# Optimization experiments

Hardware: AMD Instinct MI355X
Metric: run time of the kernel (lower is better)

Reference implementation:

```python
import jax, jax.numpy as jnp
import numpy as np

B, C, H, W = 8, 256, 64, 64
NH = 8
CM = 2048
EPS = 1e-5


def setup_inputs() -> dict:
    key = jax.random.key(0)
    ks = jax.random.split(key, 16)
    n = lambda k, s: (jax.random.normal(k, s, dtype=jnp.float32) * 0.02)
    return {
        'x': jax.random.normal(ks[0], (B, C, H, W), dtype=jnp.float32),
        'Wqkv': n(ks[1], (C, 3 * C)), 'bqkv': n(ks[2], (3 * C,)),
        'dw_w': n(ks[3], (C, 1, 3, 3)), 'dw_b': n(ks[4], (C,)),
        'Wproj': n(ks[5], (C, C)), 'bproj': n(ks[6], (C,)),
        'bn1_g': jnp.ones((C,), jnp.float32), 'bn1_b': jnp.zeros((C,), jnp.float32),
        'bn1_m': n(ks[7], (C,)), 'bn1_v': jax.random.uniform(ks[8], (C,), dtype=jnp.float32) + 0.5,
        'alpha1': jnp.ones((1,), jnp.float32),
        'Wfc1': n(ks[9], (C, CM)), 'bfc1': n(ks[10], (CM,)),
        'Wfc2': n(ks[11], (CM, C)), 'bfc2': n(ks[12], (C,)),
        'bn2_g': jnp.ones((C,), jnp.float32), 'bn2_b': jnp.zeros((C,), jnp.float32),
        'bn2_m': n(ks[13], (C,)), 'bn2_v': jax.random.uniform(ks[14], (C,), dtype=jnp.float32) + 0.5,
        'alpha2': jnp.ones((1,), jnp.float32),
    }


def _repbn(x, g, b, m, v, alpha):
    # eval-mode RepBN: BatchNorm1d with running stats over channel dim + alpha*x
    bn = (x - m) * jax.lax.rsqrt(v + EPS) * g + b
    return bn + alpha * x


def reference(x, Wqkv, bqkv, dw_w, dw_b, Wproj, bproj,
              bn1_g, bn1_b, bn1_m, bn1_v, alpha1,
              Wfc1, bfc1, Wfc2, bfc2,
              bn2_g, bn2_b, bn2_m, bn2_v, alpha2):
    b, c, h, w = x.shape
    n = h * w
    hd = c // NH
    scale = hd ** (-0.5)
    t = x.reshape(b, c, n).transpose(0, 2, 1)  # [B,N,C]

    # --- SimplifiedLinearAttention ---
    qkv = (t @ Wqkv + bqkv).reshape(b, n, 3, NH, hd).transpose(2, 0, 3, 1, 4)
    q, k, v = qkv[0], qkv[1], qkv[2]          # [B,H,N,hd]
    q = jax.nn.relu(q) * scale
    k = jax.nn.relu(k)
    ctx = jnp.einsum('bhnd,bhne->bhde', k, v)  # [B,H,hd,hd] small context
    out = jnp.einsum('bhnd,bhde->bhne', q, ctx)
    out = out.transpose(0, 2, 1, 3).reshape(b, n, c)
    img = out.transpose(0, 2, 1).reshape(b, c, h, w)
    img = jax.lax.conv_general_dilated(img, dw_w, (1, 1), 'SAME',
                                       feature_group_count=c)
    img = img + dw_b[None, :, None, None]
    out = img.reshape(b, c, n).transpose(0, 2, 1)
    out = out @ Wproj + bproj

    # residual + RepBN (eval branch of LinearNorm)
    t = _repbn(t + out, bn1_g, bn1_b, bn1_m, bn1_v, alpha1)

    # FFN (exact GELU as nn.GELU default)
    ff = jax.nn.gelu(t @ Wfc1 + bfc1, approximate=False) @ Wfc2 + bfc2
    t = _repbn(t + ff, bn2_g, bn2_b, bn2_m, bn2_v, alpha2)

    return t.transpose(0, 2, 1).reshape(b, c, h, w)
```

## Files before the change

kernel.cpp:

```cpp
#include <hip/hip_runtime.h>
#include <hip/hip_bf16.h>
#include <math.h>

constexpr int B_ = 8, C_ = 256, H_ = 64, W_ = 64;
constexpr int N_ = H_ * W_;
constexpr int NH_ = 8;
constexpr int CM_ = 2048;
constexpr int M_ = B_ * N_;
constexpr float EPS_ = 1e-5f;

typedef __bf16 bf16_t;
typedef bf16_t bf16x4 __attribute__((ext_vector_type(4)));
typedef bf16_t bf16x8 __attribute__((ext_vector_type(8)));
typedef float f32x4 __attribute__((ext_vector_type(4)));

__device__ inline bf16_t f2b(float f) {
    __hip_bfloat16 h = __float2bfloat16(f);
    return *reinterpret_cast<bf16_t*>(&h);
}
__device__ inline float b2f(bf16_t b) {
    unsigned short u = *reinterpret_cast<unsigned short*>(&b);
    unsigned int x = (unsigned int)u << 16;
    return *reinterpret_cast<float*>(&x);
}
__device__ inline unsigned pk2(float lo, float hi) {
    bf16_t l = f2b(lo), h = f2b(hi);
    unsigned short ls = *reinterpret_cast<unsigned short*>(&l);
    unsigned short hs = *reinterpret_cast<unsigned short*>(&h);
    return ((unsigned)hs << 16) | (unsigned)ls;
}
__device__ inline float gelu_ap(float y) {
    float u = y * (0.7978845608f + 0.0356774081f * y * y);
    float e = __expf(2.0f * u);
    return y - y * __builtin_amdgcn_rcpf(e + 1.0f);
}

#define GLOAD_LDS16(gptr, lptr)                                                     \
    __builtin_amdgcn_global_load_lds(                                               \
        (const __attribute__((address_space(1))) void*)(gptr),                      \
        (__attribute__((address_space(3))) void*)(lptr), 16, 0, 0)

__global__ __launch_bounds__(256)
void prep(const float* __restrict__ x, bf16_t* __restrict__ t_b,
          const float* __restrict__ Wqkv, bf16_t* __restrict__ WqkvT,
          const float* __restrict__ Wproj, bf16_t* __restrict__ WprojT,
          const float* __restrict__ Wfc1, bf16_t* __restrict__ Wfc1T,
          const float* __restrict__ Wfc2, bf16_t* __restrict__ Wfc2T) {
    __shared__ float tile[32][33];
    int id = blockIdx.x;
    int tx = threadIdx.x, ty = threadIdx.y;

    const float* src;
    bf16_t* dst;
    int K, N, k0, n0;

    if (id < 8192) {
        int b = id >> 10, rem = id & 1023;
        int nn = (rem & 127) * 32, cc = (rem >> 7) * 32;
#pragma unroll
        for (int i = ty; i < 32; i += 8)
            tile[i][tx] = x[(size_t)b * C_ * N_ + (size_t)(cc + i) * N_ + nn + tx];
        __syncthreads();
#pragma unroll
        for (int i = ty; i < 32; i += 8)
            t_b[(size_t)b * N_ * C_ + (size_t)(nn + i) * C_ + cc + tx] = f2b(tile[tx][i]);
        return;
    } else if (id < 8384) {
        int idw = id - 8192; K = C_; N = 768;
        n0 = (idw % 24) * 32; k0 = (idw / 24) * 32;
        src = Wqkv; dst = WqkvT;
    } else if (id < 8448) {
        int idw = id - 8384; K = C_; N = C_;
        n0 = (idw & 7) * 32; k0 = (idw >> 3) * 32;
        src = Wproj; dst = WprojT;
    } else if (id < 8960) {
        int idw = id - 8448; K = C_; N = CM_;
        n0 = (idw & 63) * 32; k0 = (idw >> 6) * 32;
        src = Wfc1; dst = Wfc1T;
    } else {
        int idw = id - 8960; K = CM_; N = C_;
        n0 = (idw & 7) * 32; k0 = (idw >> 3) * 32;
        src = Wfc2; dst = Wfc2T;
    }
#pragma unroll
    for (int i = ty; i < 32; i += 8)
        tile[i][tx] = src[(size_t)(k0 + i) * N + n0 + tx];
    __syncthreads();
#pragma unroll
    for (int i = ty; i < 32; i += 8)
        dst[(size_t)(n0 + i) * K + k0 + tx] = f2b(tile[tx][i]);
}

template <int EPI>
__global__ __launch_bounds__(256, 4)
void gemm_swp(const bf16_t* __restrict__ Wt, const bf16_t* __restrict__ Act,
              const float* __restrict__ bias, bf16_t* __restrict__ Cb,
              int M, int N, int K,
              const bf16_t* __restrict__ tres_b,
              const float* __restrict__ g, const float* __restrict__ bb,
              const float* __restrict__ mm, const float* __restrict__ vv,
              const float* __restrict__ alpha) {
    __shared__ bf16x8 ldsv[2048];
    char* lds = (char*)ldsv;

    int tid  = threadIdx.x;
    int lane = tid & 63;
    int w    = tid >> 6;
    int wi   = w >> 1, wj = w & 1;

    int nwg = gridDim.x * gridDim.y;
    int bid = blockIdx.y * gridDim.x + blockIdx.x;
    int swz = (bid & 7) * (nwg >> 3) + (bid >> 3);
    int bx = swz % gridDim.x, by = swz / gridDim.x;
    int bch = bx * 128, bm = by * 128;

    int rowl = lane & 15, kq = lane >> 4;

    f32x4 acc[4][4] = {};

    for (int k0 = 0; k0 < K; k0 += 64) {
#pragma unroll
        for (int j = 0; j < 4; ++j) {
            int jj = w * 4 + j;
            int msub = jj >> 1, kh = jj & 1;
            const bf16_t* gw = Wt + ((size_t)(bch + msub * 16 + rowl) * K + k0 + kh * 32 + kq * 8);
            GLOAD_LDS16(gw, lds + jj * 1024);
            const bf16_t* ga = Act + ((size_t)(bm + msub * 16 + rowl) * K + k0 + kh * 32 + kq * 8);
            GLOAD_LDS16(ga, lds + 16384 + jj * 1024);
        }
        __syncthreads();
#pragma unroll
        for (int ks = 0; ks < 2; ++ks) {
            bf16x8 wf[4], af[4];
#pragma unroll
            for (int i = 0; i < 4; ++i) wf[i] = ldsv[((wi * 4 + i) * 2 + ks) * 64 + lane];
#pragma unroll
            for (int j = 0; j < 4; ++j) af[j] = ldsv[1024 + ((wj * 4 + j) * 2 + ks) * 64 + lane];
#pragma unroll
            for (int i = 0; i < 4; ++i)
#pragma unroll
                for (int j = 0; j < 4; ++j)
                    acc[i][j] = __builtin_amdgcn_mfma_f32_16x16x32_bf16(wf[i], af[j], acc[i][j], 0, 0, 0);
        }
        __syncthreads();
    }

    float alpha_v = (EPI == 1) ? alpha[0] : 0.f;
#pragma unroll
    for (int i = 0; i < 4; ++i) {
        int ch = bch + wi * 64 + i * 16 + (lane >> 4) * 4;
        f32x4 b4 = *(const f32x4*)(bias + ch);
        f32x4 rs4, B4, m4;
        if (EPI == 1) {
            f32x4 g4 = *(const f32x4*)(g + ch);
            f32x4 v4 = *(const f32x4*)(vv + ch);
            B4 = *(const f32x4*)(bb + ch);
            m4 = *(const f32x4*)(mm + ch);
#pragma unroll
            for (int r = 0; r < 4; ++r) rs4[r] = rsqrtf(v4[r] + EPS_) * g4[r];
        }
#pragma unroll
        for (int j = 0; j < 4; ++j) {
            int m = bm + wj * 64 + j * 16 + (lane & 15);
            f32x4 a = acc[i][j];
            bf16_t ob[4];
            if (EPI == 4) {
#pragma unroll
                for (int r = 0; r < 4; ++r) ob[r] = f2b(a[r] + b4[r]);
            } else {
                bf16x4 t4 = *(const bf16x4*)(tres_b + (size_t)m * N + ch);
#pragma unroll
                for (int r = 0; r < 4; ++r) {
                    float z = b2f(t4[r]) + a[r] + b4[r];
                    ob[r] = f2b((z - m4[r]) * rs4[r] + B4[r] + alpha_v * z);
                }
            }
            *(bf16x4*)(Cb + (size_t)m * N + ch) = *(bf16x4*)ob;
        }
    }
}

__global__ __launch_bounds__(512, 4)
void ffn_fused(const bf16_t* __restrict__ Act, const bf16_t* __restrict__ W1t,
               const bf16_t* __restrict__ W2t,
               const float* __restrict__ bfc1, const float* __restrict__ bfc2,
               const float* __restrict__ g, const float* __restrict__ bb,
               const float* __restrict__ mm, const float* __restrict__ vv,
               const float* __restrict__ alpha, float* __restrict__ out) {
    __shared__ char lds[65536];
    bf16x8* ldsA = (bf16x8*)lds;

    const int tid = threadIdx.x;
    const int lane = tid & 63;
    const int w = tid >> 6;
    const int l15 = lane & 15;
    const int kq = lane >> 4;
    const int m0 = blockIdx.x * 64;

#pragma unroll
    for (int j = 0; j < 4; ++j) {
        int jj = w * 4 + j;
        int mblk = jj >> 3, ks = jj & 7;
        const bf16_t* src = Act + (size_t)(m0 + mblk * 16 + l15) * 256 + ks * 32 + kq * 8;
        GLOAD_LDS16(src, lds + jj * 1024);
    }
    __syncthreads();

    f32x4 acc2[2][4] = {};

    const int hrow = w * 16 + l15;
    const int ks2w = w >> 1;
    const int lane2 = l15 + (((2 * w + (kq >> 1)) & 3) << 4);
    const int hwoff = (kq & 1) << 3;
    const int chb = w * 32;

    bf16x8 w1f[8];
#pragma unroll
    for (int ks = 0; ks < 8; ++ks)
        w1f[ks] = *(const bf16x8*)(W1t + (size_t)hrow * 256 + ks * 32 + kq * 8);

    for (int c = 0; c < 16; ++c) {
        f32x4 acc1[4] = {};
#pragma unroll
        for (int ks = 0; ks < 8; ++ks)
#pragma unroll
            for (int mblk = 0; mblk < 4; ++mblk)
                acc1[mblk] = __builtin_amdgcn_mfma_f32_16x16x32_bf16(
                    w1f[ks], ldsA[(mblk * 8 + ks) * 64 + lane], acc1[mblk], 0, 0, 0);

        if (c + 1 < 16) {
#pragma unroll
            for (int ks = 0; ks < 8; ++ks)
                w1f[ks] = *(const bf16x8*)(W1t + (size_t)((c + 1) * 128 + hrow) * 256 + ks * 32 + kq * 8);
        }
        bf16x8 w2f[2][4];
#pragma unroll
        for (int cf = 0; cf < 2; ++cf)
#pragma unroll
            for (int ks2 = 0; ks2 < 4; ++ks2)
                w2f[cf][ks2] = *(const bf16x8*)(W2t + (size_t)(chb + cf * 16 + l15) * 2048 + c * 128 + ks2 * 32 + kq * 8);

        f32x4 b1 = *(const f32x4*)(bfc1 + c * 128 + w * 16 + kq * 4);
        char* hbase = lds + 32768 + (c & 1) * 16384;
#pragma unroll
        for (int mblk = 0; mblk < 4; ++mblk) {
            uint2 u2;
            u2.x = pk2(gelu_ap(acc1[mblk][0] + b1[0]), gelu_ap(acc1[mblk][1] + b1[1]));
            u2.y = pk2(gelu_ap(acc1[mblk][2] + b1[2]), gelu_ap(acc1[mblk][3] + b1[3]));
            *(uint2*)(hbase + (size_t)((mblk * 4 + ks2w) * 64 + lane2) * 16 + hwoff) = u2;
        }
        __syncthreads();

        bf16x8* ldsH = (bf16x8*)(lds + 32768 + (c & 1) * 16384);
#pragma unroll
        for (int mblk = 0; mblk < 4; ++mblk)
#pragma unroll
            for (int ks2 = 0; ks2 < 4; ++ks2) {
                bf16x8 hf = ldsH[(mblk * 4 + ks2) * 64 + lane];
                acc2[0][mblk] = __builtin_amdgcn_mfma_f32_16x16x32_bf16(hf, w2f[0][ks2], acc2[0][mblk], 0, 0, 0);
                acc2[1][mblk] = __builtin_amdgcn_mfma_f32_16x16x32_bf16(hf, w2f[1][ks2], acc2[1][mblk], 0, 0, 0);
            }
    }

    float alpha_v = alpha[0];
#pragma unroll
    for (int cf = 0; cf < 2; ++cf) {
        int ch = chb + cf * 16 + l15;
        float b2v = bfc2[ch];
        float rs = rsqrtf(vv[ch] + EPS_) * g[ch];
        float bbv = bb[ch], mv = mm[ch];
#pragma unroll
        for (int mblk = 0; mblk < 4; ++mblk) {
            int mbase = m0 + mblk * 16 + kq * 4;
            f32x4 o4;
#pragma unroll
            for (int r = 0; r < 4; ++r) {
                float z = b2f(Act[(size_t)(mbase + r) * 256 + ch]) + acc2[cf][mblk][r] + b2v;
                o4[r] = (z - mv) * rs + bbv + alpha_v * z;
            }
            int bi = mbase >> 12, ni = mbase & (N_ - 1);
            *(f32x4*)(out + ((size_t)bi * C_ + ch) * N_ + ni) = o4;
        }
    }
}

__global__ void ctx_partial(const bf16_t* __restrict__ qkv, float* __restrict__ ctxp) {
    __shared__ float kb[64][40];
    __shared__ float vb[64][40];
    int seg = blockIdx.x;
    int bh  = blockIdx.y;
    int b = bh >> 3, h = bh & 7;
    int tid = threadIdx.x;
    int d  = tid >> 3;
    int e0 = (tid & 7) * 4;
    int lrow = tid >> 2, lcol = (tid & 3) * 8;
    float acc[4] = {0.f, 0.f, 0.f, 0.f};
    const size_t base = (size_t)b * N_ * 768 + h * 32;
    for (int n0 = seg * 512; n0 < seg * 512 + 512; n0 += 64) {
        size_t ra = base + (size_t)(n0 + lrow) * 768 + lcol;
        bf16x8 kv8 = *(const bf16x8*)(qkv + ra + 256);
        bf16x8 vv8 = *(const bf16x8*)(qkv + ra + 512);
#pragma unroll
        for (int j = 0; j < 8; ++j) {
            kb[lrow][lcol + j] = b2f(kv8[j]);
            vb[lrow][lcol + j] = b2f(vv8[j]);
        }
        __syncthreads();
#pragma unroll
        for (int nl = 0; nl < 64; ++nl) {
            float kv = fmaxf(kb[nl][d], 0.f);
#pragma unroll
            for (int j = 0; j < 4; ++j)
                acc[j] = fmaf(kv, vb[nl][e0 + j], acc[j]);
        }
        __syncthreads();
    }
    float* o = ctxp + ((size_t)seg * 64 + bh) * 1024 + d * 32 + e0;
#pragma unroll
    for (int j = 0; j < 4; ++j) o[j] = acc[j];
}

__global__ void attn_out(const bf16_t* __restrict__ qkv, const float* __restrict__ ctxp,
                         bf16_t* __restrict__ img) {
    __shared__ float qb[64][33];
    __shared__ float cs[32][32];
    int n0 = blockIdx.x * 64;
    int bh = blockIdx.y;
    int b = bh >> 3, h = bh & 7;
    int tid = threadIdx.x;
    const float scale = 0.17677669529663687f;
    {
        f32x4 vv = (f32x4)0.f;
#pragma unroll
        for (int seg = 0; seg < 8; ++seg) {
            f32x4 t = ((const f32x4*)(ctxp + ((size_t)seg * 64 + bh) * 1024))[tid];
            vv = vv + t;
        }
        ((f32x4*)&cs[0][0])[tid] = vv;
    }
    const size_t base = (size_t)b * N_ * 768 + h * 32;
    int lrow = tid >> 2, lcol = (tid & 3) * 8;
    {
        bf16x8 q8 = *(const bf16x8*)(qkv + base + (size_t)(n0 + lrow) * 768 + lcol);
#pragma unroll
        for (int j = 0; j < 8; ++j)
            qb[lrow][lcol + j] = fmaxf(b2f(q8[j]), 0.f) * scale;
    }
    __syncthreads();
    int nl = tid & 63, ebase = tid >> 6;
    bf16_t* outp = img + ((size_t)b * C_ + h * 32) * N_ + n0 + nl;
#pragma unroll
    for (int p = 0; p < 8; ++p) {
        int e = ebase + p * 4;
        float s = 0.f;
#pragma unroll
        for (int dd = 0; dd < 32; ++dd)
            s = fmaf(qb[nl][dd], cs[dd][e], s);
        outp[(size_t)e * N_] = f2b(s);
    }
}

__global__ __launch_bounds__(256)
void dwconvT(const bf16_t* __restrict__ img, const float* __restrict__ w,
             const float* __restrict__ bias, bf16_t* __restrict__ outb) {
    __shared__ float spf[3][32][66];
    __shared__ float otile[64][33];
    int id = blockIdx.x;
    int cg = id & 7, y = (id >> 3) & 63, b = id >> 9;
    int tid = threadIdx.x;
    int c_l = tid >> 3, xg = tid & 7;
    int c = cg * 32 + c_l;
    const bf16_t* ip = img + (size_t)(b * C_ + c) * N_;
#pragma unroll
    for (int dy = 0; dy < 3; ++dy) {
        int yy = y + dy - 1;
        if (yy < 0 || yy > 63) {
#pragma unroll
            for (int j = 0; j < 8; ++j) spf[dy][c_l][xg * 8 + j] = 0.f;
        } else {
            bf16x8 v8 = *(const bf16x8*)(ip + yy * 64 + xg * 8);
#pragma unroll
            for (int j = 0; j < 8; ++j) spf[dy][c_l][xg * 8 + j] = b2f(v8[j]);
        }
    }
    float wv[9];
#pragma unroll
    for (int j = 0; j < 9; ++j) wv[j] = w[c * 9 + j];
    float bv = bias[c];
    __syncthreads();

    float o[8];
#pragma unroll
    for (int i = 0; i < 8; ++i) o[i] = bv;
#pragma unroll
    for (int dy = 0; dy < 3; ++dy)
#pragma unroll
        for (int dx = -1; dx <= 1; ++dx) {
            float wgt = wv[dy * 3 + dx + 1];
#pragma unroll
            for (int i = 0; i < 8; ++i) {
                int xx = xg * 8 + i + dx;
                float val = (xx < 0 || xx > 63) ? 0.f : spf[dy][c_l][xx];
                o[i] = fmaf(wgt, val, o[i]);
            }
        }
#pragma unroll
    for (int i = 0; i < 8; ++i) otile[xg * 8 + i][c_l] = o[i];
    __syncthreads();

    int x_o = tid >> 2, cq = tid & 3;
    bf16_t ob[8];
#pragma unroll
    for (int j = 0; j < 8; ++j) ob[j] = f2b(otile[x_o][cq * 8 + j]);
    *(bf16x8*)(outb + ((size_t)b * N_ + y * 64 + x_o) * 256 + cg * 32 + cq * 8) = *(bf16x8*)&ob[0];
}

extern "C" void kernel_launch(void* const* d_in, const int* in_sizes, int n_in,
                              void* d_out, int out_size, void* d_ws, size_t ws_size,
                              hipStream_t stream) {
    const float* x     = (const float*)d_in[0];
    const float* Wqkv  = (const float*)d_in[1];
    const float* bqkv  = (const float*)d_in[2];
    const float* dw_w  = (const float*)d_in[3];
    const float* dw_b  = (const float*)d_in[4];
    const float* Wproj = (const float*)d_in[5];
    const float* bproj = (const float*)d_in[6];
    const float* bn1_g = (const float*)d_in[7];
    const float* bn1_b = (const float*)d_in[8];
    const float* bn1_m = (const float*)d_in[9];
    const float* bn1_v = (const float*)d_in[10];
    const float* alpha1= (const float*)d_in[11];
    const float* Wfc1  = (const float*)d_in[12];
    const float* bfc1  = (const float*)d_in[13];
    const float* Wfc2  = (const float*)d_in[14];
    const float* bfc2  = (const float*)d_in[15];
    const float* bn2_g = (const float*)d_in[16];
    const float* bn2_b = (const float*)d_in[17];
    const float* bn2_m = (const float*)d_in[18];
    const float* bn2_v = (const float*)d_in[19];
    const float* alpha2= (const float*)d_in[20];
    float* out = (float*)d_out;

    char* ws = (char*)d_ws;
    bf16_t* t_b2    = (bf16_t*)(ws);
    bf16_t* WqkvT   = (bf16_t*)(ws + 16777216);
    bf16_t* WprojT  = (bf16_t*)(ws + 17170432);
    bf16_t* Wfc1T   = (bf16_t*)(ws + 17301504);
    bf16_t* Wfc2T   = (bf16_t*)(ws + 18350080);
    float*  ctxp    = (float*)(ws + 19398656);
    bf16_t* t_b     = (bf16_t*)(ws + 21757952);
    bf16_t* qkv_b   = (bf16_t*)(ws + 38535168);
    bf16_t* img_b   = (bf16_t*)(ws + 88866816);
    bf16_t* convT_b = (bf16_t*)(ws + 122421248);

    prep<<<9472, dim3(32, 8), 0, stream>>>(x, t_b, Wqkv, WqkvT, Wproj, WprojT,
                                           Wfc1, Wfc1T, Wfc2, Wfc2T);

    gemm_swp<4><<<dim3(768 / 128, M_ / 128), 256, 0, stream>>>(
        WqkvT, t_b, bqkv, qkv_b, M_, 768, C_,
        nullptr, nullptr, nullptr, nullptr, nullptr, nullptr);

    ctx_partial<<<dim3(8, B_ * NH_), 256, 0, stream>>>(qkv_b, ctxp);

    attn_out<<<dim3(N_ / 64, B_ * NH_), 256, 0, stream>>>(qkv_b, ctxp, img_b);

    dwconvT<<<B_ * 64 * 8, 256, 0, stream>>>(img_b, dw_w, dw_b, convT_b);

    gemm_swp<1><<<dim3(C_ / 128, M_ / 128), 256, 0, stream>>>(
        WprojT, convT_b, bproj, t_b2, M_, C_, C_,
        t_b, bn1_g, bn1_b, bn1_m, bn1_v, alpha1);

    ffn_fused<<<M_ / 64, 512, 0, stream>>>(
        t_b2, Wfc1T, Wfc2T, bfc1, bfc2,
        bn2_g, bn2_b, bn2_m, bn2_v, alpha2, out);
}
```

Measured before the change: 286.9 us.

## Switch FFN first GEMM to 32x32x16 MFMA with re-laid-out activation tiles

The fc1 stage of the fused FFN kernel now uses 32x32x16 bf16 MFMA instructions. Each wave computes a 32-row hidden slice by 32 tokens, instead of 16x16x32 tiles across four token blocks. The activation LDS layout, the GELU writeback indexing and the bias loads are rewritten to match the 32x32 accumulator layout. The W1 register prefetch of the next chunk is dropped in favour of per-group loads inside the loop. The larger MFMA shape is meant to cut instruction count and LDS reads per FLOP, at the cost of exposing W1 load latency and possibly raising register pressure.

```diff
diff --git a/kernel.cpp b/kernel.cpp
--- a/kernel.cpp
+++ b/kernel.cpp
@@ -13,6 +13,7 @@
 typedef bf16_t bf16x4 __attribute__((ext_vector_type(4)));
 typedef bf16_t bf16x8 __attribute__((ext_vector_type(8)));
 typedef float f32x4 __attribute__((ext_vector_type(4)));
+typedef float f32x16 __attribute__((ext_vector_type(16)));
 
 __device__ inline bf16_t f2b(float f) {
     __hip_bfloat16 h = __float2bfloat16(f);
@@ -194,45 +195,42 @@
     const int lane = tid & 63;
     const int w = tid >> 6;
     const int l15 = lane & 15;
+    const int l31 = lane & 31;
+    const int h5 = lane >> 5;
     const int kq = lane >> 4;
     const int m0 = blockIdx.x * 64;
 
 #pragma unroll
     for (int j = 0; j < 4; ++j) {
         int jj = w * 4 + j;
-        int mblk = jj >> 3, ks = jj & 7;
-        const bf16_t* src = Act + (size_t)(m0 + mblk * 16 + l15) * 256 + ks * 32 + kq * 8;
+        int mh_ = jj >> 4, ksl = jj & 15;
+        const bf16_t* src = Act + (size_t)(m0 + mh_ * 32 + l31) * 256 + ksl * 16 + h5 * 8;
         GLOAD_LDS16(src, lds + jj * 1024);
     }
     __syncthreads();
 
     f32x4 acc2[2][4] = {};
 
-    const int hrow = w * 16 + l15;
-    const int ks2w = w >> 1;
-    const int lane2 = l15 + (((2 * w + (kq >> 1)) & 3) << 4);
-    const int hwoff = (kq & 1) << 3;
+    const int hg = w >> 1;
+    const int mh = w & 1;
+    const int mblkw = mh * 2 + ((l31 >> 4) & 1);
     const int chb = w * 32;
 
-    bf16x8 w1f[8];
-#pragma unroll
-    for (int ks = 0; ks < 8; ++ks)
-        w1f[ks] = *(const bf16x8*)(W1t + (size_t)hrow * 256 + ks * 32 + kq * 8);
-
     for (int c = 0; c < 16; ++c) {
-        f32x4 acc1[4] = {};
-#pragma unroll
-        for (int ks = 0; ks < 8; ++ks)
-#pragma unroll
-            for (int mblk = 0; mblk < 4; ++mblk)
-                acc1[mblk] = __builtin_amdgcn_mfma_f32_16x16x32_bf16(
-                    w1f[ks], ldsA[(mblk * 8 + ks) * 64 + lane], acc1[mblk], 0, 0, 0);
-
-        if (c + 1 < 16) {
-#pragma unroll
-            for (int ks = 0; ks < 8; ++ks)
-                w1f[ks] = *(const bf16x8*)(W1t + (size_t)((c + 1) * 128 + hrow) * 256 + ks * 32 + kq * 8);
-        }
+        const bf16_t* w1p = W1t + (size_t)(c * 128 + hg * 32 + l31) * 256 + h5 * 8;
+        f32x16 acc1 = (f32x16)0.f;
+#pragma unroll
+        for (int grp = 0; grp < 4; ++grp) {
+            bf16x8 wl[4];
+#pragma unroll
+            for (int t = 0; t < 4; ++t)
+                wl[t] = *(const bf16x8*)(w1p + (grp * 4 + t) * 16);
+#pragma unroll
+            for (int t = 0; t < 4; ++t)
+                acc1 = __builtin_amdgcn_mfma_f32_32x32x16_bf16(
+                    wl[t], ldsA[(mh * 16 + grp * 4 + t) * 64 + lane], acc1, 0, 0, 0);
+        }
+
         bf16x8 w2f[2][4];
 #pragma unroll
         for (int cf = 0; cf < 2; ++cf)
@@ -240,14 +238,14 @@
             for (int ks2 = 0; ks2 < 4; ++ks2)
                 w2f[cf][ks2] = *(const bf16x8*)(W2t + (size_t)(chb + cf * 16 + l15) * 2048 + c * 128 + ks2 * 32 + kq * 8);
 
-        f32x4 b1 = *(const f32x4*)(bfc1 + c * 128 + w * 16 + kq * 4);
         char* hbase = lds + 32768 + (c & 1) * 16384;
 #pragma unroll
-        for (int mblk = 0; mblk < 4; ++mblk) {
+        for (int q = 0; q < 4; ++q) {
+            f32x4 b1 = *(const f32x4*)(bfc1 + c * 128 + hg * 32 + 8 * q + 4 * h5);
             uint2 u2;
-            u2.x = pk2(gelu_ap(acc1[mblk][0] + b1[0]), gelu_ap(acc1[mblk][1] + b1[1]));
-            u2.y = pk2(gelu_ap(acc1[mblk][2] + b1[2]), gelu_ap(acc1[mblk][3] + b1[3]));
-            *(uint2*)(hbase + (size_t)((mblk * 4 + ks2w) * 64 + lane2) * 16 + hwoff) = u2;
+            u2.x = pk2(gelu_ap(acc1[4 * q + 0] + b1[0]), gelu_ap(acc1[4 * q + 1] + b1[1]));
+            u2.y = pk2(gelu_ap(acc1[4 * q + 2] + b1[2]), gelu_ap(acc1[4 * q + 3] + b1[3]));
+            *(uint2*)(hbase + (size_t)(((mblkw * 4 + hg) * 64) + (l15 + (q << 4))) * 16 + h5 * 8) = u2;
         }
         __syncthreads();
 
```

Result: slower. 348.7 us (+21.5%).

## Warp-specialize fused FFN kernel into producer and consumer wave groups

Applied to the files above, without the earlier changes.

The fused FC1-GELU-FC2 kernel is split by wave role. Waves 0-3 compute FC1 plus GELU for 32 hidden units each and write the results into a double-buffered LDS tile. Waves 4-7 consume that tile for FC2 over 64 output channels each, and only they run the RepBN epilogue. The aim is to overlap the FC1 and FC2 phases across waves instead of running them serially in every wave. The cost is higher register pressure (larger per-wave accumulators and weight fragments), and the shared barriers must stay matched between the two groups.

```diff
diff --git a/kernel.cpp b/kernel.cpp
--- a/kernel.cpp
+++ b/kernel.cpp
@@ -206,80 +206,98 @@
     }
     __syncthreads();
 
-    f32x4 acc2[2][4] = {};
-
-    const int hrow = w * 16 + l15;
-    const int ks2w = w >> 1;
-    const int lane2 = l15 + (((2 * w + (kq >> 1)) & 3) << 4);
-    const int hwoff = (kq & 1) << 3;
-    const int chb = w * 32;
-
-    bf16x8 w1f[8];
-#pragma unroll
-    for (int ks = 0; ks < 8; ++ks)
-        w1f[ks] = *(const bf16x8*)(W1t + (size_t)hrow * 256 + ks * 32 + kq * 8);
-
-    for (int c = 0; c < 16; ++c) {
-        f32x4 acc1[4] = {};
-#pragma unroll
-        for (int ks = 0; ks < 8; ++ks)
+    if (w < 4) {
+        const int p = w;
+        bf16x8 w1f[2][8];
+#pragma unroll
+        for (int hs = 0; hs < 2; ++hs)
+#pragma unroll
+            for (int ks = 0; ks < 8; ++ks)
+                w1f[hs][ks] = *(const bf16x8*)(W1t + (size_t)(p * 32 + hs * 16 + l15) * 256 + ks * 32 + kq * 8);
+
+        for (int c = 0; c < 16; ++c) {
+            f32x4 acc1[2][4] = {};
+#pragma unroll
+            for (int ks = 0; ks < 8; ++ks)
+#pragma unroll
+                for (int mblk = 0; mblk < 4; ++mblk) {
+                    bf16x8 af = ldsA[(mblk * 8 + ks) * 64 + lane];
+                    acc1[0][mblk] = __builtin_amdgcn_mfma_f32_16x16x32_bf16(w1f[0][ks], af, acc1[0][mblk], 0, 0, 0);
+                    acc1[1][mblk] = __builtin_amdgcn_mfma_f32_16x16x32_bf16(w1f[1][ks], af, acc1[1][mblk], 0, 0, 0);
+                }
+            if (c + 1 < 16) {
+#pragma unroll
+                for (int hs = 0; hs < 2; ++hs)
+#pragma unroll
+                    for (int ks = 0; ks < 8; ++ks)
+                        w1f[hs][ks] = *(const bf16x8*)(W1t + (size_t)((c + 1) * 128 + p * 32 + hs * 16 + l15) * 256 + ks * 32 + kq * 8);
+            }
+            char* hbase = lds + 32768 + (c & 1) * 16384;
+#pragma unroll
+            for (int hs = 0; hs < 2; ++hs) {
+                f32x4 b1 = *(const f32x4*)(bfc1 + c * 128 + p * 32 + hs * 16 + kq * 4);
+#pragma unroll
+                for (int mblk = 0; mblk < 4; ++mblk) {
+                    uint2 u2;
+                    u2.x = pk2(gelu_ap(acc1[hs][mblk][0] + b1[0]), gelu_ap(acc1[hs][mblk][1] + b1[1]));
+                    u2.y = pk2(gelu_ap(acc1[hs][mblk][2] + b1[2]), gelu_ap(acc1[hs][mblk][3] + b1[3]));
+                    int slot = mblk * 4 + p;
+                    *(uint2*)(hbase + (size_t)slot * 1024 +
+                              (size_t)((hs * 2 + (kq >> 1)) * 16 + l15) * 16 + (kq & 1) * 8) = u2;
+                }
+            }
+            __syncthreads();
+        }
+    } else {
+        const int cw = w - 4;
+        f32x4 acc2[4][4] = {};
+        bf16x8 w2f[4][4];
+#pragma unroll
+        for (int cf = 0; cf < 4; ++cf)
+#pragma unroll
+            for (int ks2 = 0; ks2 < 4; ++ks2)
+                w2f[cf][ks2] = *(const bf16x8*)(W2t + (size_t)(cw * 64 + cf * 16 + l15) * 2048 + ks2 * 32 + kq * 8);
+
+        for (int c = 0; c < 16; ++c) {
+            __syncthreads();
+            bf16x8* ldsH = (bf16x8*)(lds + 32768 + (c & 1) * 16384);
 #pragma unroll
             for (int mblk = 0; mblk < 4; ++mblk)
-                acc1[mblk] = __builtin_amdgcn_mfma_f32_16x16x32_bf16(
-                    w1f[ks], ldsA[(mblk * 8 + ks) * 64 + lane], acc1[mblk], 0, 0, 0);
-
-        if (c + 1 < 16) {
-#pragma unroll
-            for (int ks = 0; ks < 8; ++ks)
-                w1f[ks] = *(const bf16x8*)(W1t + (size_t)((c + 1) * 128 + hrow) * 256 + ks * 32 + kq * 8);
-        }
-        bf16x8 w2f[2][4];
-#pragma unroll
-        for (int cf = 0; cf < 2; ++cf)
-#pragma unroll
-            for (int ks2 = 0; ks2 < 4; ++ks2)
-                w2f[cf][ks2] = *(const bf16x8*)(W2t + (size_t)(chb + cf * 16 + l15) * 2048 + c * 128 + ks2 * 32 + kq * 8);
-
-        f32x4 b1 = *(const f32x4*)(bfc1 + c * 128 + w * 16 + kq * 4);
-        char* hbase = lds + 32768 + (c & 1) * 16384;
-#pragma unroll
-        for (int mblk = 0; mblk < 4; ++mblk) {
-            uint2 u2;
-            u2.x = pk2(gelu_ap(acc1[mblk][0] + b1[0]), gelu_ap(acc1[mblk][1] + b1[1]));
-            u2.y = pk2(gelu_ap(acc1[mblk][2] + b1[2]), gelu_ap(acc1[mblk][3] + b1[3]));
-            *(uint2*)(hbase + (size_t)((mblk * 4 + ks2w) * 64 + lane2) * 16 + hwoff) = u2;
-        }
-        __syncthreads();
-
-        bf16x8* ldsH = (bf16x8*)(lds + 32768 + (c & 1) * 16384);
-#pragma unroll
-        for (int mblk = 0; mblk < 4; ++mblk)
-#pragma unroll
-            for (int ks2 = 0; ks2 < 4; ++ks2) {
-                bf16x8 hf = ldsH[(mblk * 4 + ks2) * 64 + lane];
-                acc2[0][mblk] = __builtin_amdgcn_mfma_f32_16x16x32_bf16(hf, w2f[0][ks2], acc2[0][mblk], 0, 0, 0);
-                acc2[1][mblk] = __builtin_amdgcn_mfma_f32_16x16x32_bf16(hf, w2f[1][ks2], acc2[1][mblk], 0, 0, 0);
-            }
-    }
-
-    float alpha_v = alpha[0];
-#pragma unroll
-    for (int cf = 0; cf < 2; ++cf) {
-        int ch = chb + cf * 16 + l15;
-        float b2v = bfc2[ch];
-        float rs = rsqrtf(vv[ch] + EPS_) * g[ch];
-        float bbv = bb[ch], mv = mm[ch];
-#pragma unroll
-        for (int mblk = 0; mblk < 4; ++mblk) {
-            int mbase = m0 + mblk * 16 + kq * 4;
-            f32x4 o4;
-#pragma unroll
-            for (int r = 0; r < 4; ++r) {
-                float z = b2f(Act[(size_t)(mbase + r) * 256 + ch]) + acc2[cf][mblk][r] + b2v;
-                o4[r] = (z - mv) * rs + bbv + alpha_v * z;
-            }
-            int bi = mbase >> 12, ni = mbase & (N_ - 1);
-            *(f32x4*)(out + ((size_t)bi * C_ + ch) * N_ + ni) = o4;
+#pragma unroll
+                for (int ks2 = 0; ks2 < 4; ++ks2) {
+                    bf16x8 hf = ldsH[(mblk * 4 + ks2) * 64 + lane];
+#pragma unroll
+                    for (int cf = 0; cf < 4; ++cf)
+                        acc2[cf][mblk] = __builtin_amdgcn_mfma_f32_16x16x32_bf16(hf, w2f[cf][ks2], acc2[cf][mblk], 0, 0, 0);
+                }
+            if (c + 1 < 16) {
+#pragma unroll
+                for (int cf = 0; cf < 4; ++cf)
+#pragma unroll
+                    for (int ks2 = 0; ks2 < 4; ++ks2)
+                        w2f[cf][ks2] = *(const bf16x8*)(W2t + (size_t)(cw * 64 + cf * 16 + l15) * 2048 + (c + 1) * 128 + ks2 * 32 + kq * 8);
+            }
+        }
+
+        float alpha_v = alpha[0];
+#pragma unroll
+        for (int cf = 0; cf < 4; ++cf) {
+            int ch = cw * 64 + cf * 16 + l15;
+            float b2v = bfc2[ch];
+            float rs = rsqrtf(vv[ch] + EPS_) * g[ch];
+            float bbv = bb[ch], mv = mm[ch];
+#pragma unroll
+            for (int mblk = 0; mblk < 4; ++mblk) {
+                int mbase = m0 + mblk * 16 + kq * 4;
+                f32x4 o4;
+#pragma unroll
+                for (int r = 0; r < 4; ++r) {
+                    float z = b2f(Act[(size_t)(mbase + r) * 256 + ch]) + acc2[cf][mblk][r] + b2v;
+                    o4[r] = (z - mv) * rs + bbv + alpha_v * z;
+                }
+                int bi = mbase >> 12, ni = mbase & (N_ - 1);
+                *(f32x4*)(out + ((size_t)bi * C_ + ch) * N_ + ni) = o4;
+            }
         }
     }
 }
```

After: 328.7 us. 14.6% more time.
